# Optimization experiments

Hardware: AMD Instinct MI355X
Metric: run time of the kernel (lower is better)

## Reference

```python
import jax, jax.numpy as jnp
import numpy as np
from jax import lax

B, KLEN, KDIM, QDIM, ADIM, VDIM = 32, 2000, 512, 512, 512, 512
CONV_CH, CONV_K = 10, 201

def setup_inputs() -> dict:
    key = jax.random.key(0)
    ks = jax.random.split(key, 16)
    s = lambda fan: 1.0 / np.sqrt(fan)
    return {
        "key": jax.random.normal(ks[0], (B, KLEN, KDIM), jnp.float32),
        "value": jax.random.normal(ks[1], (B, KLEN, VDIM), jnp.float32),
        "query": jax.random.normal(ks[2], (B, 1, QDIM), jnp.float32),
        "aw_prev": jnp.zeros((B, 1, KLEN), jnp.float32),
        "mask": jnp.ones((B, 1, KLEN), jnp.int32),
        # parameters (torch nn.Linear: y = x @ W.T + b, W is [out,in])
        "Wk": jax.random.uniform(ks[3], (ADIM, KDIM), jnp.float32, -s(KDIM), s(KDIM)),
        "bk": jax.random.uniform(ks[4], (ADIM,), jnp.float32, -s(KDIM), s(KDIM)),
        "Wq": jax.random.uniform(ks[5], (ADIM, QDIM), jnp.float32, -s(QDIM), s(QDIM)),
        "conv_w": jax.random.uniform(ks[6], (CONV_CH, 1, CONV_K), jnp.float32, -s(CONV_K), s(CONV_K)),
        "Wconv": jax.random.uniform(ks[7], (ADIM, CONV_CH), jnp.float32, -s(CONV_CH), s(CONV_CH)),
        "v": jax.random.uniform(ks[8], (ADIM,), jnp.float32, -s(ADIM), s(ADIM)),
    }

def reference(key, value, query, aw_prev, mask, Wk, bk, Wq, conv_w, Wconv, v):
    # location-aware attention, qlen == 1, sharpening_factor == 1, no dropout (eval)
    kproj = jnp.einsum('bkd,ad->bka', key, Wk) + bk              # [B, klen, adim]
    qproj = jnp.einsum('bqd,ad->bqa', query, Wq)                 # [B, 1, adim]
    # conv over previous attention weights: 1D 'same' conv, 1 -> CONV_CH channels
    conv_feat = lax.conv_general_dilated(
        aw_prev, conv_w, window_strides=(1,), padding='SAME',
        dimension_numbers=('NCH', 'OIH', 'NCH'))                 # [B, C, klen]
    conv_proj = jnp.einsum('bck,ac->bka', conv_feat, Wconv)      # [B, klen, adim]
    # additive score: v^T tanh(Wk k + Wq q + Wc f)
    tmp = jnp.tanh(kproj[:, None] + qproj[:, :, None] + conv_proj[:, None])  # [B,1,klen,adim]
    e = jnp.einsum('bqka,a->bqk', tmp, v)                        # [B, 1, klen]
    neg_inf = jnp.finfo(e.dtype).min
    e = jnp.where(mask == 0, neg_inf, e)
    aw = jax.nn.softmax(e, axis=-1)                              # [B, 1, klen]
    cv = jnp.einsum('bqk,bkv->bqv', aw, value)                   # [B, 1, vdim]
    return cv, aw[:, None]  # aw: [B, 1(H), 1(qlen), klen]
```

## Files before the change

kernel.cpp:

```cpp
#include <hip/hip_runtime.h>
#include <hip/hip_bf16.h>
#include <math.h>

#define B 32
#define KLEN 2000
#define KDIM 512
#define QDIM 512
#define ADIM 512
#define VDIM 512
#define CONV_CH 10
#define CONV_K 201
#define NROWS (B*KLEN)

#define NKS  33
#define ZERO16 {0,0,0,0,0,0,0,0,0,0,0,0,0,0,0,0}

typedef __attribute__((ext_vector_type(8)))  short bf16x8;
typedef __attribute__((ext_vector_type(16))) float f32x16;
typedef __attribute__((ext_vector_type(4)))  float f32x4;
typedef __attribute__((ext_vector_type(2)))  float f32x2;

__device__ __forceinline__ ushort f32_to_bf16(float f) {
    union { float f; unsigned int u; } v; v.f = f;
    unsigned int x = v.u;
    unsigned int r = (x + 0x7FFFu + ((x >> 16) & 1u)) >> 16;
    return (ushort)r;
}

__device__ __forceinline__ float fast_tanh(float x) {
    return 1.0f - 2.0f / (__expf(2.0f * x) + 1.0f);
}

#define MFMA32(a, bfr, c) __builtin_amdgcn_mfma_f32_32x32x16_bf16(a, bfr, c, 0, 0, 0)

__global__ void k_pack_w(const float* __restrict__ Wk, const float* __restrict__ Wconv,
                         const float* __restrict__ bk, ushort* __restrict__ wp) {
    int t = blockIdx.x * 256 + threadIdx.x;
    int lane = t & 63;
    int idx = t >> 6;
    int ks = idx % NKS, nt = idx / NKS;
    int h = lane >> 5, r = lane & 31;
    int a = nt * 32 + r;
    int j0 = ks * 16 + h * 8;
    union { uint4 v; ushort u[8]; } pk;
    #pragma unroll
    for (int jj = 0; jj < 8; jj++) {
        int j = j0 + jj;
        float val;
        if (j < 512)       val = Wk[a * KDIM + j];
        else if (j < 522)  val = Wconv[a * CONV_CH + (j - 512)];
        else if (j == 522) val = bk[a];
        else               val = 0.f;
        pk.u[jj] = f32_to_bf16(val);
    }
    *(uint4*)(wp + (size_t)t * 8) = pk.v;
}

__global__ void k_qproj(const float* __restrict__ query, const float* __restrict__ Wq,
                        float* __restrict__ qproj) {
    int t = blockIdx.x * 256 + threadIdx.x;
    int b = t >> 9, a = t & 511;
    const f32x4* q = (const f32x4*)(query + b * QDIM);
    const f32x4* w = (const f32x4*)(Wq + a * QDIM);
    float acc = 0.f;
    #pragma unroll 4
    for (int i = 0; i < 128; i++) {
        f32x4 qv = q[i], wv = w[i];
        acc += qv[0]*wv[0] + qv[1]*wv[1] + qv[2]*wv[2] + qv[3]*wv[3];
    }
    qproj[t] = acc;
}

__global__ void k_conv(const float* __restrict__ aw_prev, const float* __restrict__ conv_w,
                       float* __restrict__ cf) {
    int t = blockIdx.x * 256 + threadIdx.x;
    if (t >= B * CONV_CH * KLEN) return;
    int k = t % KLEN;
    int c = (t / KLEN) % CONV_CH;
    int b = t / (KLEN * CONV_CH);
    const float* aw = aw_prev + b * KLEN;
    const float* w  = conv_w + c * CONV_K;
    int lo = k - 100;
    int t0 = lo < 0 ? -lo : 0;
    int t1 = (lo + CONV_K > KLEN) ? (KLEN - lo) : CONV_K;
    float acc = 0.f;
    for (int tt = t0; tt < t1; tt++) acc += w[tt] * aw[lo + tt];
    cf[t] = acc;
}

__global__ __launch_bounds__(512, 4)
void k_main(const float* __restrict__ key, const ushort* __restrict__ wp,
            const float* __restrict__ qproj, const float* __restrict__ cf,
            const float* __restrict__ vvec, float* __restrict__ ep) {
    __shared__ char Alds[65536];
    const int tid = threadIdx.x;
    const int wc = tid >> 6, lane = tid & 63;
    const int r = lane & 31, h = lane >> 5;
    const int row0 = blockIdx.x * 64;

    auto build_cf = [&](int row) -> bf16x8 {
        int b = row / KLEN, kpos = row % KLEN;
        const float* cfb = cf + ((size_t)b * CONV_CH) * KLEN + kpos;
        union { bf16x8 v8; ushort u[8]; } pk;
        if (h == 0) {
            #pragma unroll
            for (int jj = 0; jj < 8; jj++) pk.u[jj] = f32_to_bf16(cfb[(size_t)jj * KLEN]);
        } else {
            pk.u[0] = f32_to_bf16(cfb[(size_t)8 * KLEN]);
            pk.u[1] = f32_to_bf16(cfb[(size_t)9 * KLEN]);
            pk.u[2] = 0x3F80;
            pk.u[3] = 0; pk.u[4] = 0; pk.u[5] = 0; pk.u[6] = 0; pk.u[7] = 0;
        }
        return pk.v8;
    };
    bf16x8 Acf0 = build_cf(row0 + r);
    bf16x8 Acf1 = build_cf(row0 + 32 + r);

    #pragma unroll
    for (int i = 0; i < 8; i++) {
        int ch = tid + i * 512;
        int arow = ch >> 6, cx = ch & 63;
        const float* kp = key + (size_t)(row0 + arow) * KDIM + cx * 8;
        f32x4 f0 = __builtin_nontemporal_load((const f32x4*)kp);
        f32x4 f1 = __builtin_nontemporal_load((const f32x4*)(kp + 4));
        union { uint4 v; ushort u[8]; } pk;
        pk.u[0] = f32_to_bf16(f0[0]); pk.u[1] = f32_to_bf16(f0[1]);
        pk.u[2] = f32_to_bf16(f0[2]); pk.u[3] = f32_to_bf16(f0[3]);
        pk.u[4] = f32_to_bf16(f1[0]); pk.u[5] = f32_to_bf16(f1[1]);
        pk.u[6] = f32_to_bf16(f1[2]); pk.u[7] = f32_to_bf16(f1[3]);
        int off = arow * 1024 + cx * 16;
        off ^= (arow & 31) << 4;
        *(uint4*)(Alds + off) = pk.v;
    }
    __syncthreads();

    const ushort* bp0 = wp + ((size_t)(wc * 2 + 0) * NKS * 64 + lane) * 8;
    const ushort* bp1 = wp + ((size_t)(wc * 2 + 1) * NKS * 64 + lane) * 8;
    const int abase0 = r * 1024 + h * 16;
    const int abase1 = abase0 + 32768;
    const int swz = r << 4;

    f32x16 c00 = ZERO16, c01 = ZERO16;
    f32x16 c10 = ZERO16, c11 = ZERO16;

    #pragma unroll 4
    for (int ks = 0; ks < 32; ks++) {
        bf16x8 a0 = *(const bf16x8*)(Alds + ((abase0 + ks * 32) ^ swz));
        bf16x8 a1 = *(const bf16x8*)(Alds + ((abase1 + ks * 32) ^ swz));
        bf16x8 b0 = *(const bf16x8*)(bp0 + ks * 512);
        bf16x8 b1 = *(const bf16x8*)(bp1 + ks * 512);
        c00 = MFMA32(a0, b0, c00); c01 = MFMA32(a0, b1, c01);
        c10 = MFMA32(a1, b0, c10); c11 = MFMA32(a1, b1, c11);
    }
    {
        bf16x8 b0 = *(const bf16x8*)(bp0 + 32 * 512);
        bf16x8 b1 = *(const bf16x8*)(bp1 + 32 * 512);
        c00 = MFMA32(Acf0, b0, c00); c01 = MFMA32(Acf0, b1, c01);
        c10 = MFMA32(Acf1, b0, c10); c11 = MFMA32(Acf1, b1, c11);
    }

    const int colb = wc * 64 + r;
    const float v0 = vvec[colb], v1 = vvec[colb + 32];
    const int blo = row0 / KLEN;
    const int bhi = (row0 + 63) / KLEN;
    const int split = (blo + 1) * KLEN;
    const float ql0 = qproj[blo * ADIM + colb],      qh0 = qproj[bhi * ADIM + colb];
    const float ql1 = qproj[blo * ADIM + colb + 32], qh1 = qproj[bhi * ADIM + colb + 32];

    float sm0[16], sm1[16];
    #pragma unroll
    for (int i = 0; i < 16; i++) {
        const int pat = (i & 3) + 8 * (i >> 2) + 4 * h;
        {
            bool hi = (row0 + pat) >= split;
            sm0[i] = fast_tanh(c00[i] + (hi ? qh0 : ql0)) * v0
                   + fast_tanh(c01[i] + (hi ? qh1 : ql1)) * v1;
        }
        {
            bool hi = (row0 + 32 + pat) >= split;
            sm1[i] = fast_tanh(c10[i] + (hi ? qh0 : ql0)) * v0
                   + fast_tanh(c11[i] + (hi ? qh1 : ql1)) * v1;
        }
    }

    #pragma unroll
    for (int i = 0; i < 16; i++) {
        float t0 = sm0[i], t1 = sm1[i];
        t0 += __shfl_xor(t0, 1);  t1 += __shfl_xor(t1, 1);
        t0 += __shfl_xor(t0, 2);  t1 += __shfl_xor(t1, 2);
        t0 += __shfl_xor(t0, 4);  t1 += __shfl_xor(t1, 4);
        t0 += __shfl_xor(t0, 8);  t1 += __shfl_xor(t1, 8);
        t0 += __shfl_xor(t0, 16); t1 += __shfl_xor(t1, 16);
        sm0[i] = t0; sm1[i] = t1;
    }
    if (r == 0) {
        float* epw = ep + (size_t)wc * NROWS;
        #pragma unroll
        for (int i = 0; i < 16; i++) {
            const int pat = (i & 3) + 8 * (i >> 2) + 4 * h;
            epw[row0 + pat]      = sm0[i];
            epw[row0 + 32 + pat] = sm1[i];
        }
    }
}

__global__ void k_softmax(const float* __restrict__ ep, const int* __restrict__ mask,
                          float* __restrict__ aw) {
    int b = blockIdx.x;
    __shared__ float se[KLEN];
    __shared__ float redm[4], reds[4];
    int tid = threadIdx.x, lane = tid & 63, wv = tid >> 6;
    for (int k = tid; k < KLEN; k += 256) {
        int idx = b * KLEN + k;
        float val = 0.f;
        #pragma unroll
        for (int p = 0; p < 8; p++) val += ep[(size_t)p * NROWS + idx];
        se[k] = mask[idx] ? val : -3.4028235e38f;
    }
    __syncthreads();
    float m = -3.4028235e38f;
    for (int k = tid; k < KLEN; k += 256) m = fmaxf(m, se[k]);
    for (int o = 32; o; o >>= 1) m = fmaxf(m, __shfl_xor(m, o));
    if (lane == 0) redm[wv] = m;
    __syncthreads();
    m = fmaxf(fmaxf(redm[0], redm[1]), fmaxf(redm[2], redm[3]));
    float s = 0.f;
    for (int k = tid; k < KLEN; k += 256) s += __expf(se[k] - m);
    for (int o = 32; o; o >>= 1) s += __shfl_xor(s, o);
    if (lane == 0) reds[wv] = s;
    __syncthreads();
    s = reds[0] + reds[1] + reds[2] + reds[3];
    float inv = 1.0f / s;
    for (int k = tid; k < KLEN; k += 256) aw[b * KLEN + k] = __expf(se[k] - m) * inv;
}

__global__ void k_cvpart(const float* __restrict__ aw, const float* __restrict__ value,
                         float* __restrict__ part) {
    int b = blockIdx.x >> 4, chunk = blockIdx.x & 15;
    int k0 = chunk * 125;
    __shared__ float sa[125];
    int tid = threadIdx.x;
    if (tid < 125) sa[tid] = aw[b * KLEN + k0 + tid];
    __syncthreads();
    const float* vp = value + ((size_t)b * KLEN + k0) * VDIM + tid * 2;
    float ax = 0.f, ay = 0.f;
    #pragma unroll 5
    for (int k = 0; k < 125; k++) {
        const f32x2 vv = __builtin_nontemporal_load((const f32x2*)(vp + (size_t)k * VDIM));
        ax += sa[k] * vv[0]; ay += sa[k] * vv[1];
    }
    f32x2 o; o[0] = ax; o[1] = ay;
    *(f32x2*)(part + ((b * 16 + chunk) * VDIM) + tid * 2) = o;
}

__global__ void k_cvreduce(const float* __restrict__ part, float* __restrict__ cv) {
    int t = blockIdx.x * 256 + threadIdx.x;
    int b = t >> 9, col = t & 511;
    float s = 0.f;
    #pragma unroll
    for (int c = 0; c < 16; c++) s += part[(b * 16 + c) * VDIM + col];
    cv[t] = s;
}

extern "C" void kernel_launch(void* const* d_in, const int* in_sizes, int n_in,
                              void* d_out, int out_size, void* d_ws, size_t ws_size,
                              hipStream_t stream) {
    const float* key     = (const float*)d_in[0];
    const float* value   = (const float*)d_in[1];
    const float* query   = (const float*)d_in[2];
    const float* aw_prev = (const float*)d_in[3];
    const int*   mask    = (const int*)d_in[4];
    const float* Wk      = (const float*)d_in[5];
    const float* bk      = (const float*)d_in[6];
    const float* Wq      = (const float*)d_in[7];
    const float* conv_w  = (const float*)d_in[8];
    const float* Wconv   = (const float*)d_in[9];
    const float* vvec    = (const float*)d_in[10];

    char* ws = (char*)d_ws;
    ushort* wp   = (ushort*)(ws + 0);
    float* qproj = (float*)(ws + 540672);
    float* cf    = (float*)(ws + 606208);
    float* ep    = (float*)(ws + 3166208);
    float* part  = (float*)(ws + 0);

    float* cv = (float*)d_out;
    float* aw = (float*)d_out + B * VDIM;

    k_pack_w  <<<132,  256, 0, stream>>>(Wk, Wconv, bk, wp);
    k_qproj   <<<64,   256, 0, stream>>>(query, Wq, qproj);
    k_conv    <<<2500, 256, 0, stream>>>(aw_prev, conv_w, cf);
    k_main    <<<1000, 512, 0, stream>>>(key, wp, qproj, cf, vvec, ep);
    k_softmax <<<B,    256, 0, stream>>>(ep, mask, aw);
    k_cvpart  <<<B*16, 256, 0, stream>>>(aw, value, part);
    k_cvreduce<<<64,   256, 0, stream>>>(part, cv);
}
```

Before: 166.2 us.

## Reduce attention scores in-block with swapped MFMA operands and fuse mask application

The main kernel now tiles per batch (32 blocks of 64 key positions each), swaps the MFMA operands so that weights form the A side, and reduces the tanh·v partial sums across all 8 waves through shared memory. It writes a single masked score per row instead of 8 partial-score planes, so the softmax kernel no longer sums 8 planes or reads the mask. The cv partial kernel uses 8 chunks with float4 loads and a two-way row split combined through LDS. The cost is an extra block-wide barrier, some padded rows in the last tile of each batch, and fewer blocks for the value reduction.

Result: faster. 157.5 us (-5.3%).

```diff
diff --git a/kernel.cpp b/kernel.cpp
--- a/kernel.cpp
+++ b/kernel.cpp
@@ -91,36 +91,22 @@
 __global__ __launch_bounds__(512, 4)
 void k_main(const float* __restrict__ key, const ushort* __restrict__ wp,
             const float* __restrict__ qproj, const float* __restrict__ cf,
-            const float* __restrict__ vvec, float* __restrict__ ep) {
+            const float* __restrict__ vvec, const int* __restrict__ mask,
+            float* __restrict__ e_out) {
     __shared__ char Alds[65536];
+    __shared__ float partsum[8][2][32];
     const int tid = threadIdx.x;
     const int wc = tid >> 6, lane = tid & 63;
     const int r = lane & 31, h = lane >> 5;
-    const int row0 = blockIdx.x * 64;
-
-    auto build_cf = [&](int row) -> bf16x8 {
-        int b = row / KLEN, kpos = row % KLEN;
-        const float* cfb = cf + ((size_t)b * CONV_CH) * KLEN + kpos;
-        union { bf16x8 v8; ushort u[8]; } pk;
-        if (h == 0) {
-            #pragma unroll
-            for (int jj = 0; jj < 8; jj++) pk.u[jj] = f32_to_bf16(cfb[(size_t)jj * KLEN]);
-        } else {
-            pk.u[0] = f32_to_bf16(cfb[(size_t)8 * KLEN]);
-            pk.u[1] = f32_to_bf16(cfb[(size_t)9 * KLEN]);
-            pk.u[2] = 0x3F80;
-            pk.u[3] = 0; pk.u[4] = 0; pk.u[5] = 0; pk.u[6] = 0; pk.u[7] = 0;
-        }
-        return pk.v8;
-    };
-    bf16x8 Acf0 = build_cf(row0 + r);
-    bf16x8 Acf1 = build_cf(row0 + 32 + r);
+    const int b = blockIdx.x >> 5;
+    const int kbase = (blockIdx.x & 31) * 64;
 
     #pragma unroll
     for (int i = 0; i < 8; i++) {
         int ch = tid + i * 512;
         int arow = ch >> 6, cx = ch & 63;
-        const float* kp = key + (size_t)(row0 + arow) * KDIM + cx * 8;
+        int kpos = kbase + arow; if (kpos >= KLEN) kpos = KLEN - 1;
+        const float* kp = key + ((size_t)b * KLEN + kpos) * KDIM + cx * 8;
         f32x4 f0 = __builtin_nontemporal_load((const f32x4*)kp);
         f32x4 f1 = __builtin_nontemporal_load((const f32x4*)(kp + 4));
         union { uint4 v; ushort u[8]; } pk;
@@ -134,10 +120,10 @@
     }
     __syncthreads();
 
-    const ushort* bp0 = wp + ((size_t)(wc * 2 + 0) * NKS * 64 + lane) * 8;
-    const ushort* bp1 = wp + ((size_t)(wc * 2 + 1) * NKS * 64 + lane) * 8;
-    const int abase0 = r * 1024 + h * 16;
-    const int abase1 = abase0 + 32768;
+    const ushort* bpW0 = wp + ((size_t)(wc * 2 + 0) * NKS * 64 + lane) * 8;
+    const ushort* bpW1 = wp + ((size_t)(wc * 2 + 1) * NKS * 64 + lane) * 8;
+    const int base_g0 = r * 1024 + h * 16;
+    const int base_g1 = base_g0 + 32768;
     const int swz = r << 4;
 
     f32x16 c00 = ZERO16, c01 = ZERO16;
@@ -145,112 +131,119 @@
 
     #pragma unroll 4
     for (int ks = 0; ks < 32; ks++) {
-        bf16x8 a0 = *(const bf16x8*)(Alds + ((abase0 + ks * 32) ^ swz));
-        bf16x8 a1 = *(const bf16x8*)(Alds + ((abase1 + ks * 32) ^ swz));
-        bf16x8 b0 = *(const bf16x8*)(bp0 + ks * 512);
-        bf16x8 b1 = *(const bf16x8*)(bp1 + ks * 512);
-        c00 = MFMA32(a0, b0, c00); c01 = MFMA32(a0, b1, c01);
-        c10 = MFMA32(a1, b0, c10); c11 = MFMA32(a1, b1, c11);
+        bf16x8 k0 = *(const bf16x8*)(Alds + ((base_g0 + ks * 32) ^ swz));
+        bf16x8 k1 = *(const bf16x8*)(Alds + ((base_g1 + ks * 32) ^ swz));
+        bf16x8 w0 = *(const bf16x8*)(bpW0 + ks * 512);
+        bf16x8 w1 = *(const bf16x8*)(bpW1 + ks * 512);
+        c00 = MFMA32(w0, k0, c00); c01 = MFMA32(w0, k1, c01);
+        c10 = MFMA32(w1, k0, c10); c11 = MFMA32(w1, k1, c11);
     }
     {
-        bf16x8 b0 = *(const bf16x8*)(bp0 + 32 * 512);
-        bf16x8 b1 = *(const bf16x8*)(bp1 + 32 * 512);
-        c00 = MFMA32(Acf0, b0, c00); c01 = MFMA32(Acf0, b1, c01);
-        c10 = MFMA32(Acf1, b0, c10); c11 = MFMA32(Acf1, b1, c11);
-    }
-
-    const int colb = wc * 64 + r;
-    const float v0 = vvec[colb], v1 = vvec[colb + 32];
-    const int blo = row0 / KLEN;
-    const int bhi = (row0 + 63) / KLEN;
-    const int split = (blo + 1) * KLEN;
-    const float ql0 = qproj[blo * ADIM + colb],      qh0 = qproj[bhi * ADIM + colb];
-    const float ql1 = qproj[blo * ADIM + colb + 32], qh1 = qproj[bhi * ADIM + colb + 32];
-
-    float sm0[16], sm1[16];
-    #pragma unroll
-    for (int i = 0; i < 16; i++) {
-        const int pat = (i & 3) + 8 * (i >> 2) + 4 * h;
-        {
-            bool hi = (row0 + pat) >= split;
-            sm0[i] = fast_tanh(c00[i] + (hi ? qh0 : ql0)) * v0
-                   + fast_tanh(c01[i] + (hi ? qh1 : ql1)) * v1;
+        auto build_ext = [&](int kpos) -> bf16x8 {
+            int kc = kpos < KLEN ? kpos : KLEN - 1;
+            const float* cfb = cf + ((size_t)b * CONV_CH) * KLEN + kc;
+            union { bf16x8 v8; ushort u[8]; } pk;
+            if (h == 0) {
+                #pragma unroll
+                for (int jj = 0; jj < 8; jj++) pk.u[jj] = f32_to_bf16(cfb[(size_t)jj * KLEN]);
+            } else {
+                pk.u[0] = f32_to_bf16(cfb[(size_t)8 * KLEN]);
+                pk.u[1] = f32_to_bf16(cfb[(size_t)9 * KLEN]);
+                pk.u[2] = 0x3F80;
+                pk.u[3] = 0; pk.u[4] = 0; pk.u[5] = 0; pk.u[6] = 0; pk.u[7] = 0;
+            }
+            return pk.v8;
+        };
+        bf16x8 x0 = build_ext(kbase + r);
+        bf16x8 x1 = build_ext(kbase + 32 + r);
+        bf16x8 w0 = *(const bf16x8*)(bpW0 + 32 * 512);
+        bf16x8 w1 = *(const bf16x8*)(bpW1 + 32 * 512);
+        c00 = MFMA32(w0, x0, c00); c01 = MFMA32(w0, x1, c01);
+        c10 = MFMA32(w1, x0, c10); c11 = MFMA32(w1, x1, c11);
+    }
+
+    const float* qb = qproj + b * ADIM + wc * 64;
+    const float* vb = vvec + wc * 64;
+    float pg0 = 0.f, pg1 = 0.f;
+    #pragma unroll
+    for (int t = 0; t < 2; t++) {
+        const f32x16 a0 = t ? c10 : c00;
+        const f32x16 a1 = t ? c11 : c01;
+        #pragma unroll
+        for (int q = 0; q < 4; q++) {
+            f32x4 qv = *(const f32x4*)(qb + t * 32 + 8 * q + 4 * h);
+            f32x4 vv = *(const f32x4*)(vb + t * 32 + 8 * q + 4 * h);
+            #pragma unroll
+            for (int j = 0; j < 4; j++) {
+                int i = 4 * q + j;
+                pg0 += fast_tanh(a0[i] + qv[j]) * vv[j];
+                pg1 += fast_tanh(a1[i] + qv[j]) * vv[j];
+            }
         }
-        {
-            bool hi = (row0 + 32 + pat) >= split;
-            sm1[i] = fast_tanh(c10[i] + (hi ? qh0 : ql0)) * v0
-                   + fast_tanh(c11[i] + (hi ? qh1 : ql1)) * v1;
+    }
+    pg0 += __shfl_xor(pg0, 32);
+    pg1 += __shfl_xor(pg1, 32);
+    if (h == 0) { partsum[wc][0][r] = pg0; partsum[wc][1][r] = pg1; }
+    __syncthreads();
+
+    if (tid < 64) {
+        int g = tid >> 5, rr = tid & 31;
+        float s = 0.f;
+        #pragma unroll
+        for (int w = 0; w < 8; w++) s += partsum[w][g][rr];
+        int kpos = kbase + g * 32 + rr;
+        if (kpos < KLEN) {
+            int idx = b * KLEN + kpos;
+            e_out[idx] = mask[idx] ? s : -3.4028235e38f;
         }
     }
-
-    #pragma unroll
-    for (int i = 0; i < 16; i++) {
-        float t0 = sm0[i], t1 = sm1[i];
-        t0 += __shfl_xor(t0, 1);  t1 += __shfl_xor(t1, 1);
-        t0 += __shfl_xor(t0, 2);  t1 += __shfl_xor(t1, 2);
-        t0 += __shfl_xor(t0, 4);  t1 += __shfl_xor(t1, 4);
-        t0 += __shfl_xor(t0, 8);  t1 += __shfl_xor(t1, 8);
-        t0 += __shfl_xor(t0, 16); t1 += __shfl_xor(t1, 16);
-        sm0[i] = t0; sm1[i] = t1;
-    }
-    if (r == 0) {
-        float* epw = ep + (size_t)wc * NROWS;
-        #pragma unroll
-        for (int i = 0; i < 16; i++) {
-            const int pat = (i & 3) + 8 * (i >> 2) + 4 * h;
-            epw[row0 + pat]      = sm0[i];
-            epw[row0 + 32 + pat] = sm1[i];
-        }
-    }
-}
-
-__global__ void k_softmax(const float* __restrict__ ep, const int* __restrict__ mask,
-                          float* __restrict__ aw) {
+}
+
+__global__ void k_softmax(const float* __restrict__ e, float* __restrict__ aw) {
     int b = blockIdx.x;
-    __shared__ float se[KLEN];
+    const float* er = e + b * KLEN;
     __shared__ float redm[4], reds[4];
     int tid = threadIdx.x, lane = tid & 63, wv = tid >> 6;
-    for (int k = tid; k < KLEN; k += 256) {
-        int idx = b * KLEN + k;
-        float val = 0.f;
-        #pragma unroll
-        for (int p = 0; p < 8; p++) val += ep[(size_t)p * NROWS + idx];
-        se[k] = mask[idx] ? val : -3.4028235e38f;
-    }
-    __syncthreads();
     float m = -3.4028235e38f;
-    for (int k = tid; k < KLEN; k += 256) m = fmaxf(m, se[k]);
+    for (int k = tid; k < KLEN; k += 256) m = fmaxf(m, er[k]);
     for (int o = 32; o; o >>= 1) m = fmaxf(m, __shfl_xor(m, o));
     if (lane == 0) redm[wv] = m;
     __syncthreads();
     m = fmaxf(fmaxf(redm[0], redm[1]), fmaxf(redm[2], redm[3]));
     float s = 0.f;
-    for (int k = tid; k < KLEN; k += 256) s += __expf(se[k] - m);
+    for (int k = tid; k < KLEN; k += 256) s += __expf(er[k] - m);
     for (int o = 32; o; o >>= 1) s += __shfl_xor(s, o);
     if (lane == 0) reds[wv] = s;
     __syncthreads();
     s = reds[0] + reds[1] + reds[2] + reds[3];
     float inv = 1.0f / s;
-    for (int k = tid; k < KLEN; k += 256) aw[b * KLEN + k] = __expf(se[k] - m) * inv;
+    for (int k = tid; k < KLEN; k += 256) aw[b * KLEN + k] = __expf(er[k] - m) * inv;
 }
 
 __global__ void k_cvpart(const float* __restrict__ aw, const float* __restrict__ value,
                          float* __restrict__ part) {
-    int b = blockIdx.x >> 4, chunk = blockIdx.x & 15;
-    int k0 = chunk * 125;
-    __shared__ float sa[125];
+    int b = blockIdx.x >> 3, chunk = blockIdx.x & 7;
+    int k0 = chunk * 250;
+    __shared__ float sa[256];
+    __shared__ f32x4 red[128];
     int tid = threadIdx.x;
-    if (tid < 125) sa[tid] = aw[b * KLEN + k0 + tid];
-    __syncthreads();
-    const float* vp = value + ((size_t)b * KLEN + k0) * VDIM + tid * 2;
-    float ax = 0.f, ay = 0.f;
+    if (tid < 250) sa[tid] = aw[b * KLEN + k0 + tid];
+    __syncthreads();
+    const int kh = tid >> 7;
+    const int col4 = (tid & 127) * 4;
+    const float* vp = value + ((size_t)b * KLEN + k0 + kh) * VDIM + col4;
+    f32x4 acc = {0.f, 0.f, 0.f, 0.f};
     #pragma unroll 5
-    for (int k = 0; k < 125; k++) {
-        const f32x2 vv = __builtin_nontemporal_load((const f32x2*)(vp + (size_t)k * VDIM));
-        ax += sa[k] * vv[0]; ay += sa[k] * vv[1];
-    }
-    f32x2 o; o[0] = ax; o[1] = ay;
-    *(f32x2*)(part + ((b * 16 + chunk) * VDIM) + tid * 2) = o;
+    for (int k = 0; k < 250; k += 2) {
+        f32x4 vv = __builtin_nontemporal_load((const f32x4*)(vp + (size_t)k * VDIM));
+        acc += vv * sa[k + kh];
+    }
+    if (kh == 1) red[tid & 127] = acc;
+    __syncthreads();
+    if (kh == 0) {
+        acc += red[tid];
+        *(f32x4*)(part + ((b * 8 + chunk) * VDIM) + col4) = acc;
+    }
 }
 
 __global__ void k_cvreduce(const float* __restrict__ part, float* __restrict__ cv) {
@@ -258,7 +251,7 @@
     int b = t >> 9, col = t & 511;
     float s = 0.f;
     #pragma unroll
-    for (int c = 0; c < 16; c++) s += part[(b * 16 + c) * VDIM + col];
+    for (int c = 0; c < 8; c++) s += part[(b * 8 + c) * VDIM + col];
     cv[t] = s;
 }
 
@@ -281,8 +274,8 @@
     ushort* wp   = (ushort*)(ws + 0);
     float* qproj = (float*)(ws + 540672);
     float* cf    = (float*)(ws + 606208);
-    float* ep    = (float*)(ws + 3166208);
-    float* part  = (float*)(ws + 0);
+    float* e     = (float*)(ws + 3166208);
+    float* part  = (float*)(ws + 3422208);
 
     float* cv = (float*)d_out;
     float* aw = (float*)d_out + B * VDIM;
@@ -290,8 +283,8 @@
     k_pack_w  <<<132,  256, 0, stream>>>(Wk, Wconv, bk, wp);
     k_qproj   <<<64,   256, 0, stream>>>(query, Wq, qproj);
     k_conv    <<<2500, 256, 0, stream>>>(aw_prev, conv_w, cf);
-    k_main    <<<1000, 512, 0, stream>>>(key, wp, qproj, cf, vvec, ep);
-    k_softmax <<<B,    256, 0, stream>>>(ep, mask, aw);
-    k_cvpart  <<<B*16, 256, 0, stream>>>(aw, value, part);
+    k_main    <<<1024, 512, 0, stream>>>(key, wp, qproj, cf, vvec, mask, e);
+    k_softmax <<<B,    256, 0, stream>>>(e, aw);
+    k_cvpart  <<<B*8,  256, 0, stream>>>(aw, value, part);
     k_cvreduce<<<64,   256, 0, stream>>>(part, cv);
 }
```
